# Optimization experiments

Hardware: AMD Instinct MI355X
Metric: run time of the kernel (lower is better)

## Reference

```python
import jax, jax.numpy as jnp
import numpy as np

B, T, H, P, F = 65536, 128, 1, 3, 3  # batch, input_length, hidden_dims, pred_var_dims, features


def setup_inputs() -> dict:
    key = jax.random.key(0)
    ks = jax.random.split(key, 8)
    return {
        "history_input": jax.random.normal(ks[0], (B, 1, T, F), dtype=jnp.float32),
        "h0": jnp.zeros((1, B, H), dtype=jnp.float32),
        "c0": jnp.zeros((1, B, H), dtype=jnp.float32),
        "target_acc": jax.random.normal(ks[1], (B, 1, F), dtype=jnp.float32),
        "W_ih": jax.random.normal(ks[2], (4 * H, F), dtype=jnp.float32) * 0.3,
        "W_hh": jax.random.normal(ks[3], (4 * H, H), dtype=jnp.float32) * 0.3,
        "b_ih": jnp.zeros((4 * H,), dtype=jnp.float32),
        "b_hh": jnp.zeros((4 * H,), dtype=jnp.float32),
        "W_mean": jax.random.normal(ks[4], (P, T * H), dtype=jnp.float32) * 0.05,
        "b_mean": jnp.zeros((P,), dtype=jnp.float32),
        "W_var": jax.random.normal(ks[5], (6, T * H), dtype=jnp.float32) * 0.05,
        "b_var": jnp.zeros((6,), dtype=jnp.float32),
    }


def _rotation_matrix(x):
    # x: [B, T, 3]; Gram-Schmidt on last three velocity vectors -> columns of R
    v1, v2, v3 = x[:, -1], x[:, -2], x[:, -3]
    b1 = v1 / jnp.linalg.norm(v1, axis=1, keepdims=True)
    a2 = v2 - jnp.sum(v2 * b1, axis=1, keepdims=True) * b1
    b2 = a2 / jnp.linalg.norm(a2, axis=1, keepdims=True)
    b3 = jnp.cross(b1, b2)
    sign = jnp.where(jnp.sum(v3 * b3, axis=1, keepdims=True) > 0, 1.0, -1.0)
    return jnp.stack([b1, b2, sign * b3], axis=-1)  # [B, 3, 3]


def _lstm(x, h0, c0, W_ih, W_hh, b_ih, b_hh):
    # x: [B, T, F]; PyTorch gate order i, f, g, o
    def step(carry, xt):
        h, c = carry
        g = xt @ W_ih.T + b_ih + h @ W_hh.T + b_hh
        i, f, gg, o = jnp.split(g, 4, axis=-1)
        c = jax.nn.sigmoid(f) * c + jax.nn.sigmoid(i) * jnp.tanh(gg)
        h = jax.nn.sigmoid(o) * jnp.tanh(c)
        return (h, c), h
    (hT, cT), outs = jax.lax.scan(step, (h0, c0), jnp.swapaxes(x, 0, 1))
    return jnp.swapaxes(outs, 0, 1), hT, cT  # [B, T, H]


def reference(history_input, h0, c0, target_acc, W_ih, W_hh, b_ih, b_hh,
              W_mean, b_mean, W_var, b_var):
    x = history_input[:, 0]                      # [B, T, 3]
    R = _rotation_matrix(x)                      # [B, 3, 3]
    rot = jnp.einsum('bji,bkj->bki', R, x)       # R^T @ x_k for each timestep

    out, hT, cT = _lstm(rot, h0[0], c0[0], W_ih, W_hh, b_ih, b_hh)
    feat = out.reshape(out.shape[0], -1)         # [B, T*H]
    means = feat @ W_mean.T + b_mean             # [B, 3]
    elements = feat @ W_var.T + b_var            # [B, 6]

    # unit-lower-triangular L (rows filled per cumsum index = [0, 1, 3])
    eye = jnp.eye(P, dtype=elements.dtype)
    lower = jnp.broadcast_to(eye, (elements.shape[0], P, P))
    lower = lower.at[:, 1, 0].set(elements[:, 0])
    lower = lower.at[:, 2, 0].set(elements[:, 1])
    lower = lower.at[:, 2, 1].set(elements[:, 2])
    dvals = jnp.exp(elements[:, 3:6])            # positive diagonal
    diag = dvals[:, None, :] * eye               # [B, 3, 3]
    sigma = lower @ diag @ jnp.swapaxes(lower, 1, 2)

    rot_target = jnp.einsum('bji,bj->bi', R, target_acc[:, 0])  # R^T @ a
    d = means - rot_target
    sigma_inv = jnp.linalg.inv(sigma)
    quad = jnp.einsum('bi,bij,bj->b', d, sigma_inv, d)
    logprob = -0.5 * dvals.sum(axis=1) - 0.5 * quad
    return -logprob.mean()
```

## Files before the change

### kernel.cpp

```cpp
#include <hip/hip_runtime.h>

#define T_STEPS 128
#define B_TOTAL 65536
#define BLOCK 256
#define NBLOCKS (B_TOTAL / BLOCK)
#define CH 16
#define NCH (T_STEPS / CH)
#define ROWF (CH * 3)
#define RSTRIDE (ROWF + 1)
#define FPT 12

#define LOG2E 1.44269504088896f

__device__ __forceinline__ float fast_rcp(float x) {
    return __builtin_amdgcn_rcpf(x);
}
__device__ __forceinline__ float fast_sigmoid(float x) {
    return fast_rcp(1.0f + __builtin_amdgcn_exp2f(-x * LOG2E));
}
__device__ __forceinline__ float fast_tanh(float x) {
    return __builtin_fmaf(-2.0f,
        fast_rcp(1.0f + __builtin_amdgcn_exp2f(x * (2.0f * LOG2E))), 1.0f);
}

__global__ __launch_bounds__(BLOCK, 1) void lstm_nll_main(
    const float* __restrict__ x,
    const float* __restrict__ h0,
    const float* __restrict__ c0,
    const float* __restrict__ target,
    const float* __restrict__ W_ih,
    const float* __restrict__ W_hh,
    const float* __restrict__ b_ih,
    const float* __restrict__ b_hh,
    const float* __restrict__ W_mean,
    const float* __restrict__ b_mean,
    const float* __restrict__ W_var,
    const float* __restrict__ b_var,
    float* __restrict__ partial)
{
    __shared__ float  lds_x[BLOCK * RSTRIDE];
    __shared__ float4 wpack4[T_STEPS * 3];
    __shared__ float  wavesum[BLOCK / 64];

    const int tid = threadIdx.x;

    for (int idx = tid; idx < T_STEPS * 3; idx += BLOCK) {
        const int t = idx / 3;
        const int k = idx - t * 3;
        float4 v;
        if (k == 0)      v = make_float4(W_mean[0*T_STEPS+t], W_mean[1*T_STEPS+t],
                                         W_mean[2*T_STEPS+t], W_var[0*T_STEPS+t]);
        else if (k == 1) v = make_float4(W_var[1*T_STEPS+t], W_var[2*T_STEPS+t],
                                         W_var[3*T_STEPS+t], W_var[4*T_STEPS+t]);
        else             v = make_float4(W_var[5*T_STEPS+t], 0.f, 0.f, 0.f);
        wpack4[idx] = v;
    }

    const int b = blockIdx.x * BLOCK + tid;
    const float* xb = x + (size_t)b * (T_STEPS * 3);

    const float v1x = xb[127*3+0], v1y = xb[127*3+1], v1z = xb[127*3+2];
    const float v2x = xb[126*3+0], v2y = xb[126*3+1], v2z = xb[126*3+2];
    const float v3x = xb[125*3+0], v3y = xb[125*3+1], v3z = xb[125*3+2];

    const float inv1 = rsqrtf(v1x*v1x + v1y*v1y + v1z*v1z);
    const float b1x = v1x*inv1, b1y = v1y*inv1, b1z = v1z*inv1;
    const float dp  = v2x*b1x + v2y*b1y + v2z*b1z;
    const float a2x = v2x - dp*b1x, a2y = v2y - dp*b1y, a2z = v2z - dp*b1z;
    const float inv2 = rsqrtf(a2x*a2x + a2y*a2y + a2z*a2z);
    const float b2x = a2x*inv2, b2y = a2y*inv2, b2z = a2z*inv2;
    float b3x = b1y*b2z - b1z*b2y;
    float b3y = b1z*b2x - b1x*b2z;
    float b3z = b1x*b2y - b1y*b2x;
    const float sgn = (v3x*b3x + v3y*b3y + v3z*b3z) > 0.0f ? 1.0f : -1.0f;
    b3x *= sgn; b3y *= sgn; b3z *= sgn;

    const float wi00 = W_ih[0], wi01 = W_ih[1],  wi02 = W_ih[2];
    const float wi10 = W_ih[3], wi11 = W_ih[4],  wi12 = W_ih[5];
    const float wi20 = W_ih[6], wi21 = W_ih[7],  wi22 = W_ih[8];
    const float wi30 = W_ih[9], wi31 = W_ih[10], wi32 = W_ih[11];
    const float wf0x = wi00*b1x + wi01*b2x + wi02*b3x;
    const float wf0y = wi00*b1y + wi01*b2y + wi02*b3y;
    const float wf0z = wi00*b1z + wi01*b2z + wi02*b3z;
    const float wf1x = wi10*b1x + wi11*b2x + wi12*b3x;
    const float wf1y = wi10*b1y + wi11*b2y + wi12*b3y;
    const float wf1z = wi10*b1z + wi11*b2z + wi12*b3z;
    const float wf2x = wi20*b1x + wi21*b2x + wi22*b3x;
    const float wf2y = wi20*b1y + wi21*b2y + wi22*b3y;
    const float wf2z = wi20*b1z + wi21*b2z + wi22*b3z;
    const float wf3x = wi30*b1x + wi31*b2x + wi32*b3x;
    const float wf3y = wi30*b1y + wi31*b2y + wi32*b3y;
    const float wf3z = wi30*b1z + wi31*b2z + wi32*b3z;
    const float wh0 = W_hh[0], wh1 = W_hh[1], wh2 = W_hh[2], wh3 = W_hh[3];
    const float bg0 = b_ih[0] + b_hh[0];
    const float bg1 = b_ih[1] + b_hh[1];
    const float bg2 = b_ih[2] + b_hh[2];
    const float bg3 = b_ih[3] + b_hh[3];

    float h = h0[b];
    float c = c0[b];
    float m0 = 0.f, m1 = 0.f, m2 = 0.f;
    float e0 = 0.f, e1 = 0.f, e2 = 0.f, e3 = 0.f, e4 = 0.f, e5 = 0.f;

    const float4* xg4 = (const float4*)(x + (size_t)blockIdx.x * BLOCK * (T_STEPS * 3));
    int ldsaddr[FPT];
    int gidx[FPT];
    #pragma unroll
    for (int j = 0; j < FPT; ++j) {
        const int f = j * BLOCK + tid;
        const int r = f / FPT;
        const int cc = f - r * FPT;
        ldsaddr[j] = r * RSTRIDE + cc * 4;
        gidx[j]    = r * (T_STEPS * 3 / 4) + cc;
    }

    float4 pre[FPT];
    #pragma unroll
    for (int j = 0; j < FPT; ++j) pre[j] = xg4[gidx[j]];

    const float* rowp = &lds_x[tid * RSTRIDE];

    for (int tc = 0; tc < NCH; ++tc) {
        __syncthreads();
        #pragma unroll
        for (int j = 0; j < FPT; ++j) {
            lds_x[ldsaddr[j] + 0] = pre[j].x;
            lds_x[ldsaddr[j] + 1] = pre[j].y;
            lds_x[ldsaddr[j] + 2] = pre[j].z;
            lds_x[ldsaddr[j] + 3] = pre[j].w;
        }
        __syncthreads();
        if (tc + 1 < NCH) {
            const int cb = (tc + 1) * FPT;
            #pragma unroll
            for (int j = 0; j < FPT; ++j) pre[j] = xg4[gidx[j] + cb];
        }

        float hbuf[CH];
        #pragma unroll
        for (int s = 0; s < CH; ++s) {
            const float xx = rowp[s*3+0], xy = rowp[s*3+1], xz = rowp[s*3+2];
            const float gi = wf0x*xx + wf0y*xy + wf0z*xz + wh0*h + bg0;
            const float gf = wf1x*xx + wf1y*xy + wf1z*xz + wh1*h + bg1;
            const float gc = wf2x*xx + wf2y*xy + wf2z*xz + wh2*h + bg2;
            const float go = wf3x*xx + wf3y*xy + wf3z*xz + wh3*h + bg3;
            const float ig = fast_sigmoid(gi);
            const float fg = fast_sigmoid(gf);
            const float tg = fast_tanh(gc);
            const float og = fast_sigmoid(go);
            c = fg * c + ig * tg;
            h = og * fast_tanh(c);
            hbuf[s] = h;
        }
        #pragma unroll
        for (int s = 0; s < CH; ++s) {
            const int t = tc * CH + s;
            const float4 w0 = wpack4[t*3+0];
            const float4 w1 = wpack4[t*3+1];
            const float4 w2 = wpack4[t*3+2];
            const float hv = hbuf[s];
            m0 += w0.x*hv; m1 += w0.y*hv; m2 += w0.z*hv;
            e0 += w0.w*hv; e1 += w1.x*hv; e2 += w1.y*hv;
            e3 += w1.z*hv; e4 += w1.w*hv; e5 += w2.x*hv;
        }
    }

    m0 += b_mean[0]; m1 += b_mean[1]; m2 += b_mean[2];
    e0 += b_var[0]; e1 += b_var[1]; e2 += b_var[2];
    e3 += b_var[3]; e4 += b_var[4]; e5 += b_var[5];

    const float dv0 = __builtin_amdgcn_exp2f(e3 * LOG2E);
    const float dv1 = __builtin_amdgcn_exp2f(e4 * LOG2E);
    const float dv2 = __builtin_amdgcn_exp2f(e5 * LOG2E);

    const float t0 = target[b*3+0], t1 = target[b*3+1], t2 = target[b*3+2];
    const float rt0 = b1x*t0 + b1y*t1 + b1z*t2;
    const float rt1 = b2x*t0 + b2y*t1 + b2z*t2;
    const float rt2 = b3x*t0 + b3y*t1 + b3z*t2;

    const float d0 = m0 - rt0, d1 = m1 - rt1, d2 = m2 - rt2;
    const float y0 = d0;
    const float y1 = d1 - e0 * y0;
    const float y2 = d2 - e1 * y0 - e2 * y1;
    const float quad = y0*y0*fast_rcp(dv0) + y1*y1*fast_rcp(dv1)
                     + y2*y2*fast_rcp(dv2);

    float contrib = 0.5f * (dv0 + dv1 + dv2) + 0.5f * quad;

    #pragma unroll
    for (int off = 32; off > 0; off >>= 1)
        contrib += __shfl_down(contrib, off, 64);
    const int lane = tid & 63, wid = tid >> 6;
    if (lane == 0) wavesum[wid] = contrib;
    __syncthreads();
    if (tid == 0) {
        float s = 0.f;
        #pragma unroll
        for (int w = 0; w < BLOCK / 64; ++w) s += wavesum[w];
        partial[blockIdx.x] = s;
    }
}

__global__ __launch_bounds__(256) void lstm_nll_finalize(
    const float* __restrict__ partial, float* __restrict__ out, int n)
{
    const int tid = threadIdx.x;
    float s = (tid < n) ? partial[tid] : 0.0f;
    #pragma unroll
    for (int off = 32; off > 0; off >>= 1)
        s += __shfl_down(s, off, 64);
    __shared__ float wavesum[4];
    const int lane = tid & 63, wid = tid >> 6;
    if (lane == 0) wavesum[wid] = s;
    __syncthreads();
    if (tid == 0) {
        out[0] = (wavesum[0] + wavesum[1] + wavesum[2] + wavesum[3]) *
                 (1.0f / (float)B_TOTAL);
    }
}

extern "C" void kernel_launch(void* const* d_in, const int* in_sizes, int n_in,
                              void* d_out, int out_size, void* d_ws, size_t ws_size,
                              hipStream_t stream) {
    const float* x      = (const float*)d_in[0];
    const float* h0     = (const float*)d_in[1];
    const float* c0     = (const float*)d_in[2];
    const float* target = (const float*)d_in[3];
    const float* W_ih   = (const float*)d_in[4];
    const float* W_hh   = (const float*)d_in[5];
    const float* b_ih   = (const float*)d_in[6];
    const float* b_hh   = (const float*)d_in[7];
    const float* W_mean = (const float*)d_in[8];
    const float* b_mean = (const float*)d_in[9];
    const float* W_var  = (const float*)d_in[10];
    const float* b_var  = (const float*)d_in[11];

    float* partial = (float*)d_ws;

    lstm_nll_main<<<NBLOCKS, BLOCK, 0, stream>>>(
        x, h0, c0, target, W_ih, W_hh, b_ih, b_hh,
        W_mean, b_mean, W_var, b_var, partial);
    lstm_nll_finalize<<<1, 256, 0, stream>>>(partial, (float*)d_out, NBLOCKS);
}
```

Before: 178.7 us.

## Pack LSTM gate math into float2 ops and merge reciprocals, shrink chunk size

Folds the -log2e scaling into the rotated input weights and computes the gate pre-activations as packed float2 FMAs. The cell and hidden updates are rewritten so the four sigmoid and tanh evaluations share two reciprocals instead of five, with a clamp on the tanh exponent to avoid overflow. The output projection accumulators are packed into float2, and the chunk size is halved with launch bounds raised to allow more occupancy. The aim is to cut VALU and transcendental instruction count on the serial recurrence. The merged-denominator form carries some overflow risk: the products of exponentials can hit inf for large gate values.

Measured after the change: 178.5 us. About the same (-0.1%).

```diff
diff --git a/kernel.cpp b/kernel.cpp
--- a/kernel.cpp
+++ b/kernel.cpp
@@ -4,26 +4,24 @@
 #define B_TOTAL 65536
 #define BLOCK 256
 #define NBLOCKS (B_TOTAL / BLOCK)
-#define CH 16
+#define CH 8
 #define NCH (T_STEPS / CH)
 #define ROWF (CH * 3)
 #define RSTRIDE (ROWF + 1)
-#define FPT 12
+#define FPT 6
 
 #define LOG2E 1.44269504088896f
+
+typedef __attribute__((ext_vector_type(2))) float f2;
 
 __device__ __forceinline__ float fast_rcp(float x) {
     return __builtin_amdgcn_rcpf(x);
 }
-__device__ __forceinline__ float fast_sigmoid(float x) {
-    return fast_rcp(1.0f + __builtin_amdgcn_exp2f(-x * LOG2E));
-}
-__device__ __forceinline__ float fast_tanh(float x) {
-    return __builtin_fmaf(-2.0f,
-        fast_rcp(1.0f + __builtin_amdgcn_exp2f(x * (2.0f * LOG2E))), 1.0f);
-}
-
-__global__ __launch_bounds__(BLOCK, 1) void lstm_nll_main(
+__device__ __forceinline__ float fast_exp2(float x) {
+    return __builtin_amdgcn_exp2f(x);
+}
+
+__global__ __launch_bounds__(BLOCK, 4) void lstm_nll_main(
     const float* __restrict__ x,
     const float* __restrict__ h0,
     const float* __restrict__ c0,
@@ -59,6 +57,8 @@
     const int b = blockIdx.x * BLOCK + tid;
     const float* xb = x + (size_t)b * (T_STEPS * 3);
 
+    const float t0 = target[b*3+0], t1 = target[b*3+1], t2 = target[b*3+2];
+
     const float v1x = xb[127*3+0], v1y = xb[127*3+1], v1z = xb[127*3+2];
     const float v2x = xb[126*3+0], v2y = xb[126*3+1], v2z = xb[126*3+2];
     const float v3x = xb[125*3+0], v3y = xb[125*3+1], v3z = xb[125*3+2];
@@ -79,28 +79,29 @@
     const float wi10 = W_ih[3], wi11 = W_ih[4],  wi12 = W_ih[5];
     const float wi20 = W_ih[6], wi21 = W_ih[7],  wi22 = W_ih[8];
     const float wi30 = W_ih[9], wi31 = W_ih[10], wi32 = W_ih[11];
-    const float wf0x = wi00*b1x + wi01*b2x + wi02*b3x;
-    const float wf0y = wi00*b1y + wi01*b2y + wi02*b3y;
-    const float wf0z = wi00*b1z + wi01*b2z + wi02*b3z;
-    const float wf1x = wi10*b1x + wi11*b2x + wi12*b3x;
-    const float wf1y = wi10*b1y + wi11*b2y + wi12*b3y;
-    const float wf1z = wi10*b1z + wi11*b2z + wi12*b3z;
-    const float wf2x = wi20*b1x + wi21*b2x + wi22*b3x;
-    const float wf2y = wi20*b1y + wi21*b2y + wi22*b3y;
-    const float wf2z = wi20*b1z + wi21*b2z + wi22*b3z;
-    const float wf3x = wi30*b1x + wi31*b2x + wi32*b3x;
-    const float wf3y = wi30*b1y + wi31*b2y + wi32*b3y;
-    const float wf3z = wi30*b1z + wi31*b2z + wi32*b3z;
-    const float wh0 = W_hh[0], wh1 = W_hh[1], wh2 = W_hh[2], wh3 = W_hh[3];
-    const float bg0 = b_ih[0] + b_hh[0];
-    const float bg1 = b_ih[1] + b_hh[1];
-    const float bg2 = b_ih[2] + b_hh[2];
-    const float bg3 = b_ih[3] + b_hh[3];
+    const float s1 = -LOG2E, s2 = -2.0f * LOG2E;
+
+    const f2 wAx = { s1*(wi00*b1x + wi01*b2x + wi02*b3x),
+                     s1*(wi10*b1x + wi11*b2x + wi12*b3x) };
+    const f2 wAy = { s1*(wi00*b1y + wi01*b2y + wi02*b3y),
+                     s1*(wi10*b1y + wi11*b2y + wi12*b3y) };
+    const f2 wAz = { s1*(wi00*b1z + wi01*b2z + wi02*b3z),
+                     s1*(wi10*b1z + wi11*b2z + wi12*b3z) };
+    const f2 wBx = { s2*(wi20*b1x + wi21*b2x + wi22*b3x),
+                     s1*(wi30*b1x + wi31*b2x + wi32*b3x) };
+    const f2 wBy = { s2*(wi20*b1y + wi21*b2y + wi22*b3y),
+                     s1*(wi30*b1y + wi31*b2y + wi32*b3y) };
+    const f2 wBz = { s2*(wi20*b1z + wi21*b2z + wi22*b3z),
+                     s1*(wi30*b1z + wi31*b2z + wi32*b3z) };
+    const f2 wAh = { s1*W_hh[0], s1*W_hh[1] };
+    const f2 wBh = { s2*W_hh[2], s1*W_hh[3] };
+    const f2 bgA = { s1*(b_ih[0] + b_hh[0]), s1*(b_ih[1] + b_hh[1]) };
+    const f2 bgB = { s2*(b_ih[2] + b_hh[2]), s1*(b_ih[3] + b_hh[3]) };
 
     float h = h0[b];
     float c = c0[b];
-    float m0 = 0.f, m1 = 0.f, m2 = 0.f;
-    float e0 = 0.f, e1 = 0.f, e2 = 0.f, e3 = 0.f, e4 = 0.f, e5 = 0.f;
+    f2 P0 = {0.f, 0.f}, P1 = {0.f, 0.f}, P2 = {0.f, 0.f}, P3 = {0.f, 0.f};
+    float e5a = 0.f;
 
     const float4* xg4 = (const float4*)(x + (size_t)blockIdx.x * BLOCK * (T_STEPS * 3));
     int ldsaddr[FPT];
@@ -139,17 +140,26 @@
         float hbuf[CH];
         #pragma unroll
         for (int s = 0; s < CH; ++s) {
-            const float xx = rowp[s*3+0], xy = rowp[s*3+1], xz = rowp[s*3+2];
-            const float gi = wf0x*xx + wf0y*xy + wf0z*xz + wh0*h + bg0;
-            const float gf = wf1x*xx + wf1y*xy + wf1z*xz + wh1*h + bg1;
-            const float gc = wf2x*xx + wf2y*xy + wf2z*xz + wh2*h + bg2;
-            const float go = wf3x*xx + wf3y*xy + wf3z*xz + wh3*h + bg3;
-            const float ig = fast_sigmoid(gi);
-            const float fg = fast_sigmoid(gf);
-            const float tg = fast_tanh(gc);
-            const float og = fast_sigmoid(go);
-            c = fg * c + ig * tg;
-            h = og * fast_tanh(c);
+            const f2 X = { rowp[s*3+0], rowp[s*3+0] };
+            const f2 Y = { rowp[s*3+1], rowp[s*3+1] };
+            const f2 Z = { rowp[s*3+2], rowp[s*3+2] };
+            const f2 H = { h, h };
+            const f2 gA = wAx*X + wAy*Y + wAz*Z + wAh*H + bgA;
+            const f2 gB = wBx*X + wBy*Y + wBz*Z + wBh*H + bgB;
+            const float u = fast_exp2(gA.x);
+            const float a = fast_exp2(gA.y);
+            const float v = fast_exp2(gB.x);
+            const float z = fast_exp2(gB.y);
+            const float U = 1.0f + u, A = 1.0f + a, V = 1.0f + v;
+            const float Q = U * V;
+            const float num = __builtin_fmaf(c, Q, (2.0f - V) * A);
+            const float den = Q * A;
+            c = num * fast_rcp(den);
+            const float wm_raw = c * (-2.0f * LOG2E);
+            const float wm = fminf(fmaxf(wm_raw, -126.0f), 126.0f);
+            const float w = fast_exp2(wm);
+            const float W = 1.0f + w;
+            h = (2.0f - W) * fast_rcp((1.0f + z) * W);
             hbuf[s] = h;
         }
         #pragma unroll
@@ -159,21 +169,29 @@
             const float4 w1 = wpack4[t*3+1];
             const float4 w2 = wpack4[t*3+2];
             const float hv = hbuf[s];
-            m0 += w0.x*hv; m1 += w0.y*hv; m2 += w0.z*hv;
-            e0 += w0.w*hv; e1 += w1.x*hv; e2 += w1.y*hv;
-            e3 += w1.z*hv; e4 += w1.w*hv; e5 += w2.x*hv;
-        }
-    }
-
-    m0 += b_mean[0]; m1 += b_mean[1]; m2 += b_mean[2];
-    e0 += b_var[0]; e1 += b_var[1]; e2 += b_var[2];
-    e3 += b_var[3]; e4 += b_var[4]; e5 += b_var[5];
-
-    const float dv0 = __builtin_amdgcn_exp2f(e3 * LOG2E);
-    const float dv1 = __builtin_amdgcn_exp2f(e4 * LOG2E);
-    const float dv2 = __builtin_amdgcn_exp2f(e5 * LOG2E);
-
-    const float t0 = target[b*3+0], t1 = target[b*3+1], t2 = target[b*3+2];
+            const f2 Hv = { hv, hv };
+            P0 += ((f2){w0.x, w0.y}) * Hv;
+            P1 += ((f2){w0.z, w0.w}) * Hv;
+            P2 += ((f2){w1.x, w1.y}) * Hv;
+            P3 += ((f2){w1.z, w1.w}) * Hv;
+            e5a += w2.x * hv;
+        }
+    }
+
+    const float m0 = P0.x + b_mean[0];
+    const float m1 = P0.y + b_mean[1];
+    const float m2 = P1.x + b_mean[2];
+    const float e0 = P1.y + b_var[0];
+    const float e1 = P2.x + b_var[1];
+    const float e2 = P2.y + b_var[2];
+    const float e3 = P3.x + b_var[3];
+    const float e4 = P3.y + b_var[4];
+    const float e5 = e5a  + b_var[5];
+
+    const float dv0 = fast_exp2(e3 * LOG2E);
+    const float dv1 = fast_exp2(e4 * LOG2E);
+    const float dv2 = fast_exp2(e5 * LOG2E);
+
     const float rt0 = b1x*t0 + b1y*t1 + b1z*t2;
     const float rt1 = b2x*t0 + b2y*t1 + b2z*t2;
     const float rt2 = b3x*t0 + b3y*t1 + b3z*t2;
```
